# Kernel optimization log

Measured on AMD Instinct MI355X. Metric: run time of the kernel, lower is better.

## Reference

```python
import jax, jax.numpy as jnp
import numpy as np

LEAK = 0.1   # LeakyReLU negative slope used by Conv2dBatchLeaky
EPS = 1e-5   # BatchNorm eps (torch default)


def conv_bn_leaky(x, w, gamma, beta, mean, var, stride, pad):
    # Conv2d(bias=False) -> BatchNorm (inference) -> LeakyReLU(0.1)
    y = jax.lax.conv_general_dilated(
        x, w, (stride, stride), [(pad, pad), (pad, pad)],
        dimension_numbers=("NCHW", "OIHW", "NCHW"))
    scale = gamma / jnp.sqrt(var + EPS)
    shift = beta - mean * scale
    y = y * scale[None, :, None, None] + shift[None, :, None, None]
    return jnp.where(y > 0, y, LEAK * y)


def reorg(x, s):
    # lightnet Reorg: exact permutation of the darknet reorg layer
    B, C, H, W = x.shape
    x = x.reshape(B, C, H // s, s, W // s, s)
    x = x.transpose(0, 3, 5, 1, 2, 4)           # (B, s, s, C, H/s, W/s)
    return x.reshape(B, s * s * C, H // s, W // s)


def setup_inputs() -> dict:
    key = jax.random.key(0)
    ks = jax.random.split(key, 13)
    B = 64
    inp = {
        "feat0": jax.random.normal(ks[0], (B, 1024, 19, 19), jnp.float32),
        "feat1": jax.random.normal(ks[1], (B, 512, 38, 38), jnp.float32),
        "w1": jax.random.normal(ks[2], (64, 512, 1, 1), jnp.float32) * 0.05,
        "g1": jax.random.uniform(ks[3], (64,), jnp.float32, 0.5, 1.5),
        "b1": jax.random.normal(ks[4], (64,), jnp.float32) * 0.1,
        "m1": jax.random.normal(ks[5], (64,), jnp.float32) * 0.1,
        "v1": jax.random.uniform(ks[6], (64,), jnp.float32, 0.5, 1.5),
        "w2": jax.random.normal(ks[7], (1024, 1280, 3, 3), jnp.float32) * 0.02,
        "g2": jax.random.uniform(ks[8], (1024,), jnp.float32, 0.5, 1.5),
        "b2": jax.random.normal(ks[9], (1024,), jnp.float32) * 0.1,
        "m2": jax.random.normal(ks[10], (1024,), jnp.float32) * 0.1,
        "v2": jax.random.uniform(ks[11], (1024,), jnp.float32, 0.5, 1.5),
        # meta_state: (num_classes=20, num_anchors*6=30, 1024+1)
        "reweight": jax.random.normal(ks[12], (20, 30, 1025), jnp.float32) * 0.05,
    }
    return inp


def reference(feat0, feat1, w1, g1, b1, m1, v1, w2, g2, b2, m2, v2, reweight):
    # layers[0]: 1x1 ConvBatchLeaky(512->64) + Reorg(2)
    x = conv_bn_leaky(feat1, w1, g1, b1, m1, v1, stride=1, pad=0)
    x = reorg(x, 2)                                  # (B, 256, 19, 19)
    # layers[1]: 3x3 ConvBatchLeaky(1280->1024), pad=1
    cat = jnp.concatenate([x, feat0], axis=1)        # (B, 1280, 19, 19)
    pre = conv_bn_leaky(cat, w2, g2, b2, m2, v2, stride=1, pad=1)  # (B,1024,19,19)
    # get_reweighted_output: per-class dynamic 1x1 conv, batched as one einsum
    cw = reweight[:, :, :-1]                         # (K=20, O=30, 1024)
    cb = reweight[:, :, -1]                          # (K, O)
    det = jnp.einsum("bchw,koc->bkohw", pre, cw) + cb[None, :, :, None, None]
    B, _, _, H, W = det.shape
    return det.reshape(B * 20, 30, H, W)
```

## Files before the change

kernel.cpp:

```cpp
#include <hip/hip_runtime.h>

typedef unsigned short u16;
typedef __attribute__((ext_vector_type(8))) __bf16 bf16x8;
typedef __attribute__((ext_vector_type(4))) float f32x4;

__device__ __forceinline__ u16 f2bf(float f) {
  union { float f; unsigned u; } v; v.f = f;
  unsigned r = v.u + 0x7fffu + ((v.u >> 16) & 1u);
  return (u16)(r >> 16);
}

__device__ __forceinline__ void gld16(const void* g, const void* l) {
  __builtin_amdgcn_global_load_lds((const __attribute__((address_space(1))) void*)g,
                                   (__attribute__((address_space(3))) void*)l, 16, 0, 0);
}

__global__ __launch_bounds__(256) void k_prep_small(
    const float* w1, const float* rw,
    const float* g1, const float* b1, const float* m1, const float* v1,
    const float* g2, const float* b2, const float* m2, const float* v2,
    u16* w1b, u16* cwt,
    float* scale1, float* shift1, float* scale2, float* shift2, float* cbf)
{
  int i = blockIdx.x * 256 + threadIdx.x;
  if (i < 32768) { w1b[i] = f2bf(w1[i]); return; }
  i -= 32768;
  if (i < 655360) {
    int n = i >> 10, c = i & 1023;
    cwt[i] = (n < 600) ? f2bf(rw[n * 1025 + c]) : (u16)0;
    return;
  }
  i -= 655360;
  if (i < 64) {
    float s = g1[i] * rsqrtf(v1[i] + 1e-5f);
    scale1[i] = s; shift1[i] = b1[i] - m1[i] * s;
  } else if (i < 1088) {
    int c = i - 64;
    float s = g2[c] * rsqrtf(v2[c] + 1e-5f);
    scale2[c] = s; shift2[c] = b2[c] - m2[c] * s;
  } else if (i < 1728) {
    int n = i - 1088;
    cbf[n] = (n < 600) ? rw[n * 1025 + 1024] : 0.f;
  }
}

__global__ __launch_bounds__(256) void k_prep_w2(const float* w2, u16* w2t) {
  __shared__ float buf[11520];
  int o = blockIdx.x;
  const float* src = w2 + (size_t)o * 11520;
  for (int i = threadIdx.x; i < 11520; i += 256) buf[i] = src[i];
  __syncthreads();
  for (int t = 0; t < 9; ++t) {
    int dy = t / 3, dx = t - dy * 3;
    u16* dst = w2t + ((size_t)dy * 1024 + o) * 3840 + dx * 1280;
    for (int ci = threadIdx.x; ci < 1280; ci += 256) dst[ci] = f2bf(buf[ci * 9 + t]);
  }
}

__global__ __launch_bounds__(256) void k_feat0(const float* feat0, u16* cat) {
  __shared__ float tile[32][33];
  int b = blockIdx.z, c0 = blockIdx.y * 32, p0 = blockIdx.x * 32;
  int tid = threadIdx.x;
  int lo = tid & 31, hi = tid >> 5;
#pragma unroll
  for (int pass = 0; pass < 4; ++pass) {
    int cl = pass * 8 + hi;
    int p = p0 + lo;
    tile[cl][lo] = (p < 361) ? feat0[((size_t)(b * 1024 + c0 + cl)) * 361 + p] : 0.f;
  }
  __syncthreads();
#pragma unroll
  for (int pass = 0; pass < 4; ++pass) {
    int pl = pass * 8 + hi;
    int p = p0 + pl;
    if (p < 361) {
      int h = p / 19, w = p - h * 19;
      cat[(((size_t)b * 21 + 1 + h) * 21 + 1 + w) * 1280 + 256 + c0 + lo] = f2bf(tile[lo][pl]);
    }
  }
}

__global__ __launch_bounds__(256) void k_conv1(const float* feat1, const u16* w1b,
    const float* scale1, const float* shift1, u16* cat)
{
  __shared__ u16 As[128 * 40];
  __shared__ u16 Bs[64 * 32];
  int tid = threadIdx.x;
  int wave = tid >> 6, lane = tid & 63;
  int wr = wave >> 1, wc = wave & 1;
  int lm = lane & 15, lq = lane >> 4;
  int m0 = blockIdx.x * 128;

  int mLoc = tid & 127, cHalf = tid >> 7;
  int mA = m0 + mLoc;
  int bA = mA / 1444, qA = mA - bA * 1444;
  const float* aG = feat1 + ((size_t)bA * 512) * 1444 + qA;

  const u16* bG = w1b + (tid >> 2) * 512 + (tid & 3) * 8;
  char* BsW = (char*)Bs + wave * 1024;

  f32x4 acc[4][2];
#pragma unroll
  for (int i = 0; i < 4; ++i)
#pragma unroll
    for (int j = 0; j < 2; ++j)
#pragma unroll
      for (int r = 0; r < 4; ++r) acc[i][j][r] = 0.f;

  for (int k0 = 0; k0 < 512; k0 += 32) {
    gld16(bG + k0, BsW);
#pragma unroll
    for (int pass = 0; pass < 16; ++pass) {
      int c = pass * 2 + cHalf;
      As[mLoc * 40 + c] = f2bf(aG[(size_t)(k0 + c) * 1444]);
    }
    __syncthreads();
    bf16x8 aF[4], bF[2];
#pragma unroll
    for (int i = 0; i < 4; ++i)
      aF[i] = *(const bf16x8*)(As + (wr * 64 + i * 16 + lm) * 40 + lq * 8);
#pragma unroll
    for (int j = 0; j < 2; ++j)
      bF[j] = *(const bf16x8*)(Bs + (wc * 32 + j * 16 + lm) * 32 + lq * 8);
#pragma unroll
    for (int i = 0; i < 4; ++i)
#pragma unroll
      for (int j = 0; j < 2; ++j)
        acc[i][j] = __builtin_amdgcn_mfma_f32_16x16x32_bf16(aF[i], bF[j], acc[i][j], 0, 0, 0);
    __syncthreads();
  }

  int o0 = wc * 32;
  float sc[2], sh[2];
#pragma unroll
  for (int j = 0; j < 2; ++j) {
    int o = o0 + j * 16 + lm;
    sc[j] = scale1[o]; sh[j] = shift1[o];
  }
#pragma unroll
  for (int i = 0; i < 4; ++i) {
#pragma unroll
    for (int r = 0; r < 4; ++r) {
      int m = m0 + wr * 64 + i * 16 + lq * 4 + r;
      int b = m / 1444, q = m - b * 1444;
      int yy = q / 38, xx = q - yy * 38;
      size_t base = (((size_t)b * 21 + 1 + (yy >> 1)) * 21 + 1 + (xx >> 1)) * 1280
                  + ((yy & 1) * 2 + (xx & 1)) * 64;
#pragma unroll
      for (int j = 0; j < 2; ++j) {
        float v = acc[i][j][r] * sc[j] + sh[j];
        v = v > 0.f ? v : 0.1f * v;
        cat[base + o0 + j * 16 + lm] = f2bf(v);
      }
    }
  }
}

__global__ __launch_bounds__(256) void k_conv2(const u16* cat, const u16* w2t,
    const float* scale2, const float* shift2, u16* pre)
{
  __shared__ u16 As[8192];
  __shared__ u16 Bs[8192];
  int tid = threadIdx.x;
  int wave = tid >> 6, lane = tid & 63;
  int wr = wave >> 1, wc = wave & 1;
  int lm = lane & 15, lq = lane >> 4;
  int n0 = (blockIdx.x & 7) * 128;
  int m0 = (blockIdx.x >> 3) * 128;

  int rIn = lane >> 2;
  int kseg = (lane & 3) * 8;
  int rowLo = wave * 16 + rIn;

  int mLo = m0 + rowLo;       if (mLo > 23103) mLo = 23103;
  int mHi = m0 + rowLo + 64;  if (mHi > 23103) mHi = 23103;
  int bL = mLo / 361, pL = mLo - bL * 361, yL = pL / 19, xL = pL - yL * 19;
  int bH = mHi / 361, pH = mHi - bH * 361, yH = pH / 19, xH = pH - yH * 19;
  const u16* aLo = cat + ((size_t)(bL * 21 + yL) * 21 + xL) * 1280 + kseg;
  const u16* aHi = cat + ((size_t)(bH * 21 + yH) * 21 + xH) * 1280 + kseg;
  const u16* bLo = w2t + (size_t)(n0 + rowLo) * 3840 + kseg;
  const u16* bHi = bLo + (size_t)64 * 3840;

  u16* asJ0 = As + wave * 512;          u16* asJ1 = As + (4 + wave) * 512;
  u16* asJ2 = As + 4096 + wave * 512;   u16* asJ3 = As + 4096 + (4 + wave) * 512;
  u16* bsJ0 = Bs + wave * 512;          u16* bsJ1 = Bs + (4 + wave) * 512;
  u16* bsJ2 = Bs + 4096 + wave * 512;   u16* bsJ3 = Bs + 4096 + (4 + wave) * 512;

  f32x4 acc[4][4];
#pragma unroll
  for (int i = 0; i < 4; ++i)
#pragma unroll
    for (int j = 0; j < 4; ++j)
#pragma unroll
      for (int r = 0; r < 4; ++r) acc[i][j][r] = 0.f;

  for (int dy = 0; dy < 3; ++dy) {
    const u16* a0 = aLo + dy * 26880;
    const u16* a1 = aHi + dy * 26880;
    const u16* b0 = bLo + (size_t)dy * 3932160;
    const u16* b1 = bHi + (size_t)dy * 3932160;
    for (int k0 = 0; k0 < 3840; k0 += 64) {
      gld16(a0 + k0,      asJ0);
      gld16(a1 + k0,      asJ1);
      gld16(a0 + k0 + 32, asJ2);
      gld16(a1 + k0 + 32, asJ3);
      gld16(b0 + k0,      bsJ0);
      gld16(b1 + k0,      bsJ1);
      gld16(b0 + k0 + 32, bsJ2);
      gld16(b1 + k0 + 32, bsJ3);
      __syncthreads();
#pragma unroll
      for (int kk = 0; kk < 2; ++kk) {
        bf16x8 aF[4], bF[4];
#pragma unroll
        for (int i = 0; i < 4; ++i)
          aF[i] = *(const bf16x8*)(As + kk * 4096 + (wr * 64 + i * 16 + lm) * 32 + lq * 8);
#pragma unroll
        for (int j = 0; j < 4; ++j)
          bF[j] = *(const bf16x8*)(Bs + kk * 4096 + (wc * 64 + j * 16 + lm) * 32 + lq * 8);
#pragma unroll
        for (int i = 0; i < 4; ++i)
#pragma unroll
          for (int j = 0; j < 4; ++j)
            acc[i][j] = __builtin_amdgcn_mfma_f32_16x16x32_bf16(aF[i], bF[j], acc[i][j], 0, 0, 0);
      }
      __syncthreads();
    }
  }

  int nn[4]; float sc[4], sh[4];
#pragma unroll
  for (int j = 0; j < 4; ++j) {
    nn[j] = n0 + wc * 64 + j * 16 + lm;
    sc[j] = scale2[nn[j]]; sh[j] = shift2[nn[j]];
  }
#pragma unroll
  for (int i = 0; i < 4; ++i) {
#pragma unroll
    for (int r = 0; r < 4; ++r) {
      int m = m0 + wr * 64 + i * 16 + lq * 4 + r;
      if (m < 23104) {
        u16* row = pre + (size_t)m * 1024;
#pragma unroll
        for (int j = 0; j < 4; ++j) {
          float v = acc[i][j][r] * sc[j] + sh[j];
          v = v > 0.f ? v : 0.1f * v;
          row[nn[j]] = f2bf(v);
        }
      }
    }
  }
}

__global__ __launch_bounds__(256) void k_einsum(const u16* pre, const u16* cwt,
    const float* cbf, float* out)
{
  __shared__ u16 As[4096];
  __shared__ u16 Bs[4096];
  int tid = threadIdx.x;
  int wave = tid >> 6, lane = tid & 63;
  int wr = wave >> 1, wc = wave & 1;
  int lm = lane & 15, lq = lane >> 4;
  int m0 = blockIdx.x * 128;
  int n0 = blockIdx.y * 128;

  int r0 = tid >> 2, seg = (tid & 3) * 8;
  const u16* aP0 = cwt + (size_t)(m0 + r0) * 1024 + seg;
  const u16* aP1 = aP0 + (size_t)64 * 1024;
  int q0 = n0 + r0;       if (q0 > 23103) q0 = 23103;
  int q1 = n0 + r0 + 64;  if (q1 > 23103) q1 = 23103;
  const u16* bP0 = pre + (size_t)q0 * 1024 + seg;
  const u16* bP1 = pre + (size_t)q1 * 1024 + seg;

  char* AsW = (char*)As + wave * 1024;
  char* BsW = (char*)Bs + wave * 1024;

  f32x4 acc[4][4];
#pragma unroll
  for (int i = 0; i < 4; ++i)
#pragma unroll
    for (int j = 0; j < 4; ++j)
#pragma unroll
      for (int r = 0; r < 4; ++r) acc[i][j][r] = 0.f;

  for (int k0 = 0; k0 < 1024; k0 += 32) {
    gld16(aP0 + k0, AsW);
    gld16(aP1 + k0, AsW + 4096);
    gld16(bP0 + k0, BsW);
    gld16(bP1 + k0, BsW + 4096);
    __syncthreads();
    bf16x8 aF[4], bF[4];
#pragma unroll
    for (int i = 0; i < 4; ++i)
      aF[i] = *(const bf16x8*)(As + (wr * 64 + i * 16 + lm) * 32 + lq * 8);
#pragma unroll
    for (int j = 0; j < 4; ++j)
      bF[j] = *(const bf16x8*)(Bs + (wc * 64 + j * 16 + lm) * 32 + lq * 8);
#pragma unroll
    for (int i = 0; i < 4; ++i)
#pragma unroll
      for (int j = 0; j < 4; ++j)
        acc[i][j] = __builtin_amdgcn_mfma_f32_16x16x32_bf16(aF[i], bF[j], acc[i][j], 0, 0, 0);
    __syncthreads();
  }

  int pix[4], pb[4], pp[4];
#pragma unroll
  for (int j = 0; j < 4; ++j) {
    pix[j] = n0 + wc * 64 + j * 16 + lm;
    int b = pix[j] / 361;
    pb[j] = b; pp[j] = pix[j] - b * 361;
  }
#pragma unroll
  for (int i = 0; i < 4; ++i) {
#pragma unroll
    for (int r = 0; r < 4; ++r) {
      int cw = m0 + wr * 64 + i * 16 + lq * 4 + r;
      if (cw < 600) {
        float bias = cbf[cw];
#pragma unroll
        for (int j = 0; j < 4; ++j) {
          if (pix[j] < 23104)
            out[(size_t)pb[j] * 216600 + (size_t)cw * 361 + pp[j]] = acc[i][j][r] + bias;
        }
      }
    }
  }
}


extern "C" void kernel_launch(void* const* d_in, const int* in_sizes, int n_in,
                              void* d_out, int out_size, void* d_ws, size_t ws_size,
                              hipStream_t stream) {
  const float* feat0 = (const float*)d_in[0];
  const float* feat1 = (const float*)d_in[1];
  const float* w1 = (const float*)d_in[2];
  const float* g1 = (const float*)d_in[3];
  const float* b1 = (const float*)d_in[4];
  const float* m1 = (const float*)d_in[5];
  const float* v1 = (const float*)d_in[6];
  const float* w2 = (const float*)d_in[7];
  const float* g2 = (const float*)d_in[8];
  const float* b2 = (const float*)d_in[9];
  const float* m2 = (const float*)d_in[10];
  const float* v2 = (const float*)d_in[11];
  const float* rw = (const float*)d_in[12];
  float* out = (float*)d_out;

  char* ws = (char*)d_ws;
  u16* cat    = (u16*)(ws);
  u16* w2t    = (u16*)(ws + 72253440);
  u16* pre    = (u16*)(ws + 95846400);
  u16* w1b    = (u16*)(ws + 143163392);
  u16* cwt    = (u16*)(ws + 143228928);
  float* scale1 = (float*)(ws + 144539648);
  float* shift1 = (float*)(ws + 144539904);
  float* scale2 = (float*)(ws + 144540160);
  float* shift2 = (float*)(ws + 144544256);
  float* cbf    = (float*)(ws + 144548352);

  hipMemsetAsync(cat, 0, 72253440, stream);

  k_prep_small<<<2696, 256, 0, stream>>>(w1, rw, g1, b1, m1, v1, g2, b2, m2, v2,
                                         w1b, cwt, scale1, shift1, scale2, shift2, cbf);
  k_prep_w2<<<1024, 256, 0, stream>>>(w2, w2t);
  k_feat0<<<dim3(12, 32, 64), 256, 0, stream>>>(feat0, cat);
  k_conv1<<<722, 256, 0, stream>>>(feat1, w1b, scale1, shift1, cat);
  k_conv2<<<1448, 256, 0, stream>>>(cat, w2t, scale2, shift2, pre);
  k_einsum<<<dim3(5, 181), 256, 0, stream>>>(pre, cwt, cbf, out);
}
```

Baseline: 1.218 ms.

## Rework conv2 GEMM into 8-wave 256x128 tile with double-buffered swizzled LDS pipeline

The implicit-GEMM conv2 kernel now runs 512 threads per block on a 256x128 output tile with a 64-wide K step, replacing the 256-thread 128x128 tile. Loads into LDS are double-buffered, with prefetch two stages ahead under explicit vmcnt waits. LDS columns are XOR-swizzled to avoid bank conflicts, and MFMA work is split into four quadrant phases separated by barriers and setprio, so fragment loads and global prefetches overlap with compute. The costs are more LDS per block (96KB), more barriers per iteration, and fewer blocks in the grid.

```diff
diff --git a/kernel.cpp b/kernel.cpp
--- a/kernel.cpp
+++ b/kernel.cpp
@@ -14,6 +14,11 @@
   __builtin_amdgcn_global_load_lds((const __attribute__((address_space(1))) void*)g,
                                    (__attribute__((address_space(3))) void*)l, 16, 0, 0);
 }
+
+#define BARX() do { asm volatile("" ::: "memory"); __builtin_amdgcn_s_barrier(); \
+                    asm volatile("" ::: "memory"); } while (0)
+#define LGKM0() do { asm volatile("s_waitcnt lgkmcnt(0)" ::: "memory"); \
+                     __builtin_amdgcn_sched_barrier(0); } while (0)
 
 __global__ __launch_bounds__(256) void k_prep_small(
     const float* w1, const float* rw,
@@ -156,35 +161,38 @@
   }
 }
 
-__global__ __launch_bounds__(256) void k_conv2(const u16* cat, const u16* w2t,
+__global__ __launch_bounds__(512) void k_conv2(const u16* cat, const u16* w2t,
     const float* scale2, const float* shift2, u16* pre)
 {
-  __shared__ u16 As[8192];
-  __shared__ u16 Bs[8192];
+  __shared__ __align__(16) u16 As[2][16384];
+  __shared__ __align__(16) u16 Bs[2][8192];
+
   int tid = threadIdx.x;
   int wave = tid >> 6, lane = tid & 63;
   int wr = wave >> 1, wc = wave & 1;
   int lm = lane & 15, lq = lane >> 4;
   int n0 = (blockIdx.x & 7) * 128;
-  int m0 = (blockIdx.x >> 3) * 128;
-
-  int rIn = lane >> 2;
-  int kseg = (lane & 3) * 8;
-  int rowLo = wave * 16 + rIn;
-
-  int mLo = m0 + rowLo;       if (mLo > 23103) mLo = 23103;
-  int mHi = m0 + rowLo + 64;  if (mHi > 23103) mHi = 23103;
-  int bL = mLo / 361, pL = mLo - bL * 361, yL = pL / 19, xL = pL - yL * 19;
-  int bH = mHi / 361, pH = mHi - bH * 361, yH = pH / 19, xH = pH - yH * 19;
-  const u16* aLo = cat + ((size_t)(bL * 21 + yL) * 21 + xL) * 1280 + kseg;
-  const u16* aHi = cat + ((size_t)(bH * 21 + yH) * 21 + xH) * 1280 + kseg;
-  const u16* bLo = w2t + (size_t)(n0 + rowLo) * 3840 + kseg;
-  const u16* bHi = bLo + (size_t)64 * 3840;
-
-  u16* asJ0 = As + wave * 512;          u16* asJ1 = As + (4 + wave) * 512;
-  u16* asJ2 = As + 4096 + wave * 512;   u16* asJ3 = As + 4096 + (4 + wave) * 512;
-  u16* bsJ0 = Bs + wave * 512;          u16* bsJ1 = Bs + (4 + wave) * 512;
-  u16* bsJ2 = Bs + 4096 + wave * 512;   u16* bsJ3 = Bs + 4096 + (4 + wave) * 512;
+  int m0 = (blockIdx.x >> 3) * 256;
+
+  int rsub = tid >> 3;
+  int cOff = ((tid & 7) ^ (rsub & 7)) * 8;
+
+  const u16* aBase[4];
+#pragma unroll
+  for (int r = 0; r < 4; ++r) {
+    int m = m0 + r * 64 + rsub; if (m > 23103) m = 23103;
+    int b = m / 361, pq = m - b * 361, y = pq / 19, x = pq - y * 19;
+    aBase[r] = cat + ((size_t)(b * 21 + y) * 21 + x) * 1280 + cOff;
+  }
+  const u16* bBase[2];
+#pragma unroll
+  for (int r = 0; r < 2; ++r)
+    bBase[r] = w2t + (size_t)(n0 + r * 64 + rsub) * 3840 + cOff;
+
+  int c0 = ((0 + lq) ^ (lm & 7)) * 8;
+  int c1 = ((4 + lq) ^ (lm & 7)) * 8;
+  const u16* aRd = &As[0][(wr * 64 + lm) * 64];
+  const u16* bRd = &Bs[0][(wc * 64 + lm) * 64];
 
   f32x4 acc[4][4];
 #pragma unroll
@@ -194,37 +202,114 @@
 #pragma unroll
       for (int r = 0; r < 4; ++r) acc[i][j][r] = 0.f;
 
-  for (int dy = 0; dy < 3; ++dy) {
-    const u16* a0 = aLo + dy * 26880;
-    const u16* a1 = aHi + dy * 26880;
-    const u16* b0 = bLo + (size_t)dy * 3932160;
-    const u16* b1 = bHi + (size_t)dy * 3932160;
-    for (int k0 = 0; k0 < 3840; k0 += 64) {
-      gld16(a0 + k0,      asJ0);
-      gld16(a1 + k0,      asJ1);
-      gld16(a0 + k0 + 32, asJ2);
-      gld16(a1 + k0 + 32, asJ3);
-      gld16(b0 + k0,      bsJ0);
-      gld16(b1 + k0,      bsJ1);
-      gld16(b0 + k0 + 32, bsJ2);
-      gld16(b1 + k0 + 32, bsJ3);
-      __syncthreads();
-#pragma unroll
-      for (int kk = 0; kk < 2; ++kk) {
-        bf16x8 aF[4], bF[4];
-#pragma unroll
-        for (int i = 0; i < 4; ++i)
-          aF[i] = *(const bf16x8*)(As + kk * 4096 + (wr * 64 + i * 16 + lm) * 32 + lq * 8);
-#pragma unroll
-        for (int j = 0; j < 4; ++j)
-          bF[j] = *(const bf16x8*)(Bs + kk * 4096 + (wc * 64 + j * 16 + lm) * 32 + lq * 8);
-#pragma unroll
-        for (int i = 0; i < 4; ++i)
-#pragma unroll
-          for (int j = 0; j < 4; ++j)
-            acc[i][j] = __builtin_amdgcn_mfma_f32_16x16x32_bf16(aF[i], bF[j], acc[i][j], 0, 0, 0);
-      }
-      __syncthreads();
+  auto stageA = [&](int p, int aOff) {
+#pragma unroll
+    for (int r = 0; r < 4; ++r)
+      gld16(aBase[r] + aOff, &As[p][r * 4096 + wave * 512]);
+  };
+  auto stageB = [&](int p, size_t bOff) {
+#pragma unroll
+    for (int r = 0; r < 2; ++r)
+      gld16(bBase[r] + bOff, &Bs[p][r * 4096 + wave * 512]);
+  };
+
+  stageA(0, 0);        stageB(0, 0);
+  stageA(1, 64);       stageB(1, 64);
+  asm volatile("s_waitcnt vmcnt(6)" ::: "memory");
+  __builtin_amdgcn_sched_barrier(0);
+  BARX();
+
+  int dyS = 0, koS = 128;
+
+  for (int kt = 0; kt < 180; ++kt) {
+    int p = kt & 1;
+    const u16* A = aRd + p * 16384;
+    const u16* B = bRd + p * 8192;
+    bool pf = (kt + 2 < 180);
+    int aOff = dyS * 26880 + koS;
+    size_t bOff = (size_t)dyS * 3932160 + koS;
+
+    bf16x8 aF[4][2], bF[4][2];
+
+#pragma unroll
+    for (int i = 0; i < 2; ++i) {
+      aF[i][0] = *(const bf16x8*)(A + i * 1024 + c0);
+      aF[i][1] = *(const bf16x8*)(A + i * 1024 + c1);
+    }
+#pragma unroll
+    for (int j = 0; j < 2; ++j) {
+      bF[j][0] = *(const bf16x8*)(B + j * 1024 + c0);
+      bF[j][1] = *(const bf16x8*)(B + j * 1024 + c1);
+    }
+    BARX();
+    LGKM0();
+    __builtin_amdgcn_s_setprio(1);
+#pragma unroll
+    for (int i = 0; i < 2; ++i)
+#pragma unroll
+      for (int j = 0; j < 2; ++j) {
+        acc[i][j] = __builtin_amdgcn_mfma_f32_16x16x32_bf16(aF[i][0], bF[j][0], acc[i][j], 0, 0, 0);
+        acc[i][j] = __builtin_amdgcn_mfma_f32_16x16x32_bf16(aF[i][1], bF[j][1], acc[i][j], 0, 0, 0);
+      }
+    __builtin_amdgcn_s_setprio(0);
+    BARX();
+
+#pragma unroll
+    for (int i = 2; i < 4; ++i) {
+      aF[i][0] = *(const bf16x8*)(A + i * 1024 + c0);
+      aF[i][1] = *(const bf16x8*)(A + i * 1024 + c1);
+    }
+    BARX();
+    LGKM0();
+    __builtin_amdgcn_s_setprio(1);
+#pragma unroll
+    for (int i = 2; i < 4; ++i)
+#pragma unroll
+      for (int j = 0; j < 2; ++j) {
+        acc[i][j] = __builtin_amdgcn_mfma_f32_16x16x32_bf16(aF[i][0], bF[j][0], acc[i][j], 0, 0, 0);
+        acc[i][j] = __builtin_amdgcn_mfma_f32_16x16x32_bf16(aF[i][1], bF[j][1], acc[i][j], 0, 0, 0);
+      }
+    __builtin_amdgcn_s_setprio(0);
+    BARX();
+
+#pragma unroll
+    for (int j = 2; j < 4; ++j) {
+      bF[j][0] = *(const bf16x8*)(B + j * 1024 + c0);
+      bF[j][1] = *(const bf16x8*)(B + j * 1024 + c1);
+    }
+    if (pf) stageA(p, aOff);
+    BARX();
+    LGKM0();
+    __builtin_amdgcn_s_setprio(1);
+#pragma unroll
+    for (int i = 2; i < 4; ++i)
+#pragma unroll
+      for (int j = 2; j < 4; ++j) {
+        acc[i][j] = __builtin_amdgcn_mfma_f32_16x16x32_bf16(aF[i][0], bF[j][0], acc[i][j], 0, 0, 0);
+        acc[i][j] = __builtin_amdgcn_mfma_f32_16x16x32_bf16(aF[i][1], bF[j][1], acc[i][j], 0, 0, 0);
+      }
+    __builtin_amdgcn_s_setprio(0);
+    BARX();
+
+    if (pf) stageB(p, bOff);
+    __builtin_amdgcn_s_setprio(1);
+#pragma unroll
+    for (int i = 0; i < 2; ++i)
+#pragma unroll
+      for (int j = 2; j < 4; ++j) {
+        acc[i][j] = __builtin_amdgcn_mfma_f32_16x16x32_bf16(aF[i][0], bF[j][0], acc[i][j], 0, 0, 0);
+        acc[i][j] = __builtin_amdgcn_mfma_f32_16x16x32_bf16(aF[i][1], bF[j][1], acc[i][j], 0, 0, 0);
+      }
+    __builtin_amdgcn_s_setprio(0);
+
+    koS += 64;
+    if (koS == 3840) { koS = 0; ++dyS; }
+
+    if (kt < 179) {
+      if (kt == 178) { asm volatile("s_waitcnt vmcnt(0)" ::: "memory"); }
+      else           { asm volatile("s_waitcnt vmcnt(6)" ::: "memory"); }
+      __builtin_amdgcn_sched_barrier(0);
+      BARX();
     }
   }
 
@@ -366,6 +451,6 @@
   k_prep_w2<<<1024, 256, 0, stream>>>(w2, w2t);
   k_feat0<<<dim3(12, 32, 64), 256, 0, stream>>>(feat0, cat);
   k_conv1<<<722, 256, 0, stream>>>(feat1, w1b, scale1, shift1, cat);
-  k_conv2<<<1448, 256, 0, stream>>>(cat, w2t, scale2, shift2, pre);
+  k_conv2<<<728, 512, 0, stream>>>(cat, w2t, scale2, shift2, pre);
   k_einsum<<<dim3(5, 181), 256, 0, stream>>>(pre, cwt, cbf, out);
 }
```

New measurement: 1.308 ms. +7.3%, slower.
